# Performance work log

Measured on AMD Instinct MI355X. Metric: run time of the kernel, lower is better.

The kernel has to match this reference:

```python
import jax, jax.numpy as jnp
import numpy as np

B, N, C_IN, C_OUT, K = 8, 4096, 64, 128, 15
RADIUS = 0.1            # 2.5 * grid_size(0.04) * sigma(1.0)
MAX_NN = 34
KP_EXTENT = 0.04        # point_influence = prev_grid_size * sigma
KERNEL_RADIUS = 1.5 * KP_EXTENT
NEG_SLOPE = 0.2
BN_EPS = 1e-5


def setup_inputs() -> dict:
    key = jax.random.key(0)
    k1, k2, k3, k4 = jax.random.split(key, 4)
    xyz = jax.random.uniform(k1, (B, N, 3), dtype=jnp.float32)
    feats = jax.random.normal(k2, (B, N, C_IN), dtype=jnp.float32)
    # fixed kernel point disposition inside the kernel ball (requires_grad=False in torch)
    kp = jax.random.normal(k3, (K, 3), dtype=jnp.float32)
    kp = kp / (jnp.linalg.norm(kp, axis=-1, keepdims=True) + 1e-6) * KERNEL_RADIUS * 0.7
    kp = kp.at[0].set(0.0)  # center point
    std = float(np.sqrt(2.0 / (K * C_IN)))
    weight = jax.random.normal(k4, (K, C_IN, C_OUT), dtype=jnp.float32) * std
    gamma = jnp.ones((C_OUT,), dtype=jnp.float32)
    beta = jnp.zeros((C_OUT,), dtype=jnp.float32)
    return {"xyz": xyz, "feats": feats, "K_points": kp, "weight": weight,
            "gamma": gamma, "beta": beta}


def _ball_query(xyz):
    # xyz: [B, N, 3] -> flat neighbor idx [B*N, MAX_NN] into the concatenated
    # point array; missing neighbors get shadow index B*N.
    b_, n_, _ = xyz.shape
    shadow = b_ * n_

    def per_cloud(pts, b):
        d2 = jnp.sum((pts[:, None, :] - pts[None, :, :]) ** 2, axis=-1)  # [N, N]
        neg_d2, idx = jax.lax.top_k(-d2, MAX_NN)                         # k nearest
        valid = (-neg_d2) <= RADIUS ** 2
        return jnp.where(valid, idx + b * n_, shadow)

    return jax.vmap(per_cloud)(xyz, jnp.arange(b_)).reshape(b_ * n_, MAX_NN)


def _kpconv_block(xyz, feats, K_points, weight, gamma, beta):
    b_, n_, _ = xyz.shape
    pts = xyz.reshape(b_ * n_, 3)
    f = feats.reshape(b_ * n_, C_IN)
    nidx = _ball_query(xyz)                                   # [M, nn]
    # shadow point far away / zero features (KPConv_ops)
    pts_pad = jnp.concatenate([pts, jnp.full((1, 3), 1e6, pts.dtype)], axis=0)
    f_pad = jnp.concatenate([f, jnp.zeros((1, C_IN), f.dtype)], axis=0)
    nbr = pts_pad[nidx] - pts[:, None, :]                     # [M, nn, 3] relative coords
    sq = jnp.sum((nbr[:, :, None, :] - K_points) ** 2, -1)    # [M, nn, K]
    w = jnp.maximum(1.0 - jnp.sqrt(sq) / KP_EXTENT, 0.0)      # linear influence
    nf = f_pad[nidx]                                          # [M, nn, Cin]
    wf = jnp.einsum('mnk,mnc->mkc', w, nf)                    # per-kernel-point feats
    out = jnp.einsum('mkc,kcd->md', wf, weight)               # [M, Cout]
    # FastBatchNorm1d (training-mode batch stats, biased var) + LeakyReLU
    mu = out.mean(axis=0)
    var = out.var(axis=0)
    out = (out - mu) * jax.lax.rsqrt(var + BN_EPS) * gamma + beta
    out = jnp.where(out >= 0, out, NEG_SLOPE * out)
    return out.reshape(b_, n_, C_OUT)


def reference(xyz, feats, K_points, weight, gamma, beta):
    return _kpconv_block(xyz, feats, K_points, weight, gamma, beta)
```

## Files before the change

kernel.cpp:

```cpp
#include <hip/hip_runtime.h>


#define NB     8
#define NPTS   4096
#define M_TOT  32768
#define CIN    64
#define COUT   128
#define NKP    15
#define NCELL  1728
#define UCAP   400
#define R2EFF  (0.082f * 0.082f)
#define KP_INV 25.0f
#define NEG_SLOPE 0.2f
#define KCP    960
#define WFROW  1920
#define SP     40

typedef float f32x4_t __attribute__((ext_vector_type(4)));
typedef short bf16x8_t __attribute__((ext_vector_type(8)));

__device__ __forceinline__ unsigned short f2bf(float f) {
  union { float f; unsigned u; } v; v.f = f;
  unsigned r = v.u + 0x7FFF + ((v.u >> 16) & 1);
  return (unsigned short)(r >> 16);
}
__device__ __forceinline__ unsigned short f2bf_fast(float f) {
  union { float f; unsigned u; } v; v.f = f;
  return (unsigned short)((v.u + 0x8000u) >> 16);
}
__device__ __forceinline__ int cell_of(float x, float y, float z) {
  int cx = (int)(x * 12.f); cx = cx > 11 ? 11 : cx;
  int cy = (int)(y * 12.f); cy = cy > 11 ? 11 : cy;
  int cz = (int)(z * 12.f); cz = cz > 11 ? 11 : cz;
  return (cz * 12 + cy) * 12 + cx;
}

__global__ __launch_bounds__(256) void k0a_hist(
    const float* __restrict__ xyz, int* __restrict__ cellcnt)
{
  const int pt = blockIdx.x * 256 + threadIdx.x;
  const float x = xyz[pt * 3], y = xyz[pt * 3 + 1], z = xyz[pt * 3 + 2];
  const int b = pt >> 12;
  atomicAdd(&cellcnt[b * NCELL + cell_of(x, y, z)], 1);
}

__global__ __launch_bounds__(256) void k0b_scan_kW(
    const int* __restrict__ cellcnt, int* __restrict__ cellstart,
    const float* __restrict__ W, unsigned short* __restrict__ Wt)
{
  if (blockIdx.x >= 8) {
    const int idx = (blockIdx.x - 8) * 256 + threadIdx.x;
    const int c = idx & 63, d = idx >> 6;
    #pragma unroll
    for (int k = 0; k < NKP; k++)
      Wt[(size_t)d * KCP + k * 64 + c] =
          f2bf(W[(size_t)k * (CIN * COUT) + c * COUT + d]);
    return;
  }
  __shared__ int ps[256];
  const int b = blockIdx.x, t = threadIdx.x;
  int local[7], s = 0;
  #pragma unroll
  for (int i = 0; i < 7; i++) {
    const int cid = t * 7 + i;
    const int c = (cid < NCELL) ? cellcnt[b * NCELL + cid] : 0;
    local[i] = c; s += c;
  }
  ps[t] = s; __syncthreads();
  for (int off = 1; off < 256; off <<= 1) {
    int v = (t >= off) ? ps[t - off] : 0;
    __syncthreads();
    ps[t] += v;
    __syncthreads();
  }
  int run = ps[t] - s;
  #pragma unroll
  for (int i = 0; i < 7; i++) {
    const int cid = t * 7 + i;
    if (cid < NCELL) { cellstart[b * 1729 + cid] = run; run += local[i]; }
  }
  if (t == 255) cellstart[b * 1729 + NCELL] = ps[255];
}

__global__ __launch_bounds__(256) void k0c_scatter(
    const float* __restrict__ xyz, const float* __restrict__ feats,
    const int* __restrict__ cellstart, int* __restrict__ cellfill,
    int* __restrict__ qorder, float4* __restrict__ xyzs,
    unsigned short* __restrict__ fsorted)
{
  const int pt = blockIdx.x * 256 + threadIdx.x;
  const float x = xyz[pt * 3], y = xyz[pt * 3 + 1], z = xyz[pt * 3 + 2];
  const int b = pt >> 12;
  const int cid = cell_of(x, y, z);
  const int slot = atomicAdd(&cellfill[b * NCELL + cid], 1);
  const int pos = b * NPTS + cellstart[b * 1729 + cid] + slot;
  qorder[pos] = pt;
  xyzs[pos] = make_float4(x, y, z, 0.f);
  const float* src = &feats[(size_t)pt * CIN];
  uint4* dst = (uint4*)&fsorted[(size_t)pos * CIN];
  #pragma unroll
  for (int g = 0; g < 8; g++) {
    float4 a = *(const float4*)(src + g * 8);
    float4 c = *(const float4*)(src + g * 8 + 4);
    union { unsigned short s[8]; uint4 v; } u;
    u.s[0] = f2bf(a.x); u.s[1] = f2bf(a.y); u.s[2] = f2bf(a.z); u.s[3] = f2bf(a.w);
    u.s[4] = f2bf(c.x); u.s[5] = f2bf(c.y); u.s[6] = f2bf(c.z); u.s[7] = f2bf(c.w);
    dst[g] = u.v;
  }
}

__global__ __launch_bounds__(256, 5) void k2_conv(
    const float4* __restrict__ xyzs, const unsigned short* __restrict__ fsorted,
    const float* __restrict__ kpts, const int* __restrict__ cellstart,
    const int* __restrict__ qorder, const unsigned short* __restrict__ Wt,
    float* __restrict__ out, float* __restrict__ psum,
    float* __restrict__ psumsq)
{
  __shared__ char smraw[32000] __attribute__((aligned(16)));
  float4*         Pu   = (float4*)smraw;
  unsigned short* cpos = (unsigned short*)(smraw + 6400);
  short (*S)[SP]       = (short(*)[SP])(smraw + 6400);
  short (*FT)[SP]      = (short(*)[SP])(smraw + 26880);

  __shared__ float4 qd[16];
  __shared__ int    qm[16];
  __shared__ float  kp[NKP][4];
  __shared__ int    Tsh;
  __shared__ int    ucnt;

  const int tid = threadIdx.x;
  const int w   = tid >> 6;
  const int L   = tid & 63;
  const int m0  = blockIdx.x * 16;
  const int b   = m0 >> 12;

  if (tid >= 64 && tid < 64 + NKP) {
    const int k = tid - 64;
    const float kx = kpts[k * 3], ky = kpts[k * 3 + 1], kz = kpts[k * 3 + 2];
    kp[k][0] = -2.f * kx; kp[k][1] = -2.f * ky; kp[k][2] = -2.f * kz;
    kp[k][3] = kx * kx + ky * ky + kz * kz;
  }

  if (tid < 64) {
    int cxm = 12, cym = 12, czm = 12, cxM = -1, cyM = -1, czM = -1;
    if (tid < 16) {
      const float4 Q = xyzs[m0 + tid];
      qd[tid] = Q;
      qm[tid] = qorder[m0 + tid];
      int a = (int)(Q.x * 12.f); a = a > 11 ? 11 : a;
      int c = (int)(Q.y * 12.f); c = c > 11 ? 11 : c;
      int d = (int)(Q.z * 12.f); d = d > 11 ? 11 : d;
      cxm = cxM = a; cym = cyM = c; czm = czM = d;
    }
    #pragma unroll
    for (int off = 8; off >= 1; off >>= 1) {
      int v;
      v = __shfl_xor(cxm, off); cxm = v < cxm ? v : cxm;
      v = __shfl_xor(cxM, off); cxM = v > cxM ? v : cxM;
      v = __shfl_xor(cym, off); cym = v < cym ? v : cym;
      v = __shfl_xor(cyM, off); cyM = v > cyM ? v : cyM;
      v = __shfl_xor(czm, off); czm = v < czm ? v : czm;
      v = __shfl_xor(czM, off); czM = v > czM ? v : czM;
    }
    cxm = __shfl(cxm, 0); cxM = __shfl(cxM, 0);
    cym = __shfl(cym, 0); cyM = __shfl(cyM, 0);
    czm = __shfl(czm, 0); czM = __shfl(czM, 0);

    const int x0 = cxm > 0 ? cxm - 1 : 0, x1 = cxM < 11 ? cxM + 1 : 11;
    const int y0 = cym > 0 ? cym - 1 : 0, y1 = cyM < 11 ? cyM + 1 : 11;
    const int z0 = czm > 0 ? czm - 1 : 0, z1 = czM < 11 ? czM + 1 : 11;
    const int yspan = y1 - y0 + 1;
    int nr = yspan * (z1 - z0 + 1);
    nr = nr > 64 ? 64 : nr;

    int rs = 0, len = 0;
    if (tid < nr) {
      const int zz = z0 + tid / yspan, yy = y0 + tid % yspan;
      const int base = b * 1729 + (zz * 12 + yy) * 12;
      rs  = cellstart[base + x0];
      len = cellstart[base + x1 + 1] - rs;
    }
    int incl = len;
    #pragma unroll
    for (int off = 1; off < 64; off <<= 1) {
      const int v = __shfl_up(incl, off);
      if (tid >= off) incl += v;
    }
    const int excl = incl - len;
    for (int i = 0; i < len; i++) cpos[excl + i] = (unsigned short)(rs + i);
    if (tid == 63) Tsh = incl;
    if (tid == 62) ucnt = 0;
  }
  __syncthreads();
  const int T = Tsh;

  for (int tb = 0; tb < T; tb += 256) {
    const int t = tb + tid;
    if (t < T) {
      const int pos = (int)cpos[t];
      const float4 P = xyzs[b * NPTS + pos];
      float best = 1e9f;
      #pragma unroll
      for (int i = 0; i < 16; i++) {
        const float4 Q = qd[i];
        const float dx = P.x - Q.x, dy = P.y - Q.y, dz = P.z - Q.z;
        const float d2 = dx * dx + dy * dy + dz * dz;
        best = d2 < best ? d2 : best;
      }
      if (best <= R2EFF) {
        const int slot = atomicAdd(&ucnt, 1);
        if (slot < UCAP)
          Pu[slot] = make_float4(P.x, P.y, P.z, __int_as_float(pos));
      }
    }
  }
  __syncthreads();
  int U = ucnt; U = U > UCAP ? UCAP : U;

  const int ln = L & 15;
  const int kh = L >> 4;
  const int qh = tid >> 5;
  const int nn = tid & 31;

  f32x4_t acc[16];
  #pragma unroll
  for (int mt = 0; mt < 16; mt++) acc[mt] = (f32x4_t){0.f, 0.f, 0.f, 0.f};

  for (int ub = 0; ub < U; ub += 32) {
    {
      const int c  = tid & 63;
      const int i0 = tid >> 6;
      #pragma unroll
      for (int ii = 0; ii < 8; ii++) {
        const int i = ii * 4 + i0;
        const int u = ub + i;
        short v = 0;
        if (u < U) {
          const int pos = __float_as_int(Pu[u].w);
          v = (short)fsorted[(size_t)(b * NPTS + pos) * CIN + c];
        }
        FT[c][i] = v;
      }
    }

    bf16x8_t bb;
    #pragma unroll
    for (int half = 0; half < 2; half++) {
      {
        const int u = ub + nn;
        if (u < U) {
          const float4 P = Pu[u];
          const float4 Q = qd[half * 8 + qh];
          const float rx = P.x - Q.x, ry = P.y - Q.y, rz = P.z - Q.z;
          const float rr = rx * rx + ry * ry + rz * rz;
          #pragma unroll
          for (int k = 0; k < NKP; k++) {
            float d2 = fmaf(kp[k][0], rx,
                       fmaf(kp[k][1], ry,
                       fmaf(kp[k][2], rz, rr + kp[k][3])));
            d2 = fmaxf(d2, 0.f);
            const float wv =
                fmaxf(fmaf(-KP_INV, __builtin_amdgcn_sqrtf(d2), 1.f), 0.f);
            S[qh * 16 + k][nn] = (short)f2bf_fast(wv);
          }
          S[qh * 16 + 15][nn] = 0;
        } else {
          #pragma unroll
          for (int k = 0; k < 16; k++) S[qh * 16 + k][nn] = 0;
        }
      }
      __syncthreads();
      if (half == 0) bb = *(const bf16x8_t*)&FT[w * 16 + ln][kh * 8];
      #pragma unroll
      for (int mt = 0; mt < 8; mt++) {
        bf16x8_t aa = *(const bf16x8_t*)&S[mt * 16 + ln][kh * 8];
        acc[half * 8 + mt] =
            __builtin_amdgcn_mfma_f32_16x16x32_bf16(aa, bb, acc[half * 8 + mt],
                                                    0, 0, 0);
      }
      __syncthreads();
    }
  }

  {
    const int c = w * 16 + ln;
    #pragma unroll
    for (int mt = 0; mt < 16; mt++) {
      #pragma unroll
      for (int j = 0; j < 4; j++) {
        const int k = kh * 4 + j;
        if (k < 15) {
          int byteo = mt * WFROW + ((k * 64 + c) << 1);
          byteo ^= (mt & 7) << 4;
          *(unsigned short*)(smraw + byteo) = f2bf_fast(acc[mt][j]);
        }
      }
    }
  }
  __syncthreads();

  const int colbase = w * 32;

  f32x4_t acc2[2];
  acc2[0] = (f32x4_t){0.f, 0.f, 0.f, 0.f};
  acc2[1] = (f32x4_t){0.f, 0.f, 0.f, 0.f};

  const unsigned short* Bp0 = &Wt[(size_t)(colbase + ln) * KCP + kh * 8];
  const unsigned short* Bp1 = Bp0 + 16 * KCP;
  const char* wfb = (const char*)smraw + ln * WFROW;
  const int   sw  = (ln & 7) << 4;

  #pragma unroll 6
  for (int kk = 0; kk < 30; kk++) {
    const int ko  = kk * 32;
    const int inr = (kh * 16 + kk * 64) ^ sw;
    bf16x8_t b0 = *(const bf16x8_t*)(Bp0 + ko);
    bf16x8_t b1 = *(const bf16x8_t*)(Bp1 + ko);
    bf16x8_t a0 = *(const bf16x8_t*)(wfb + inr);
    acc2[0] = __builtin_amdgcn_mfma_f32_16x16x32_bf16(a0, b0, acc2[0], 0, 0, 0);
    acc2[1] = __builtin_amdgcn_mfma_f32_16x16x32_bf16(a0, b1, acc2[1], 0, 0, 0);
  }

  float s0 = 0.f, q0 = 0.f, s1 = 0.f, q1 = 0.f;
  #pragma unroll
  for (int j = 0; j < 4; j++) {
    s0 += acc2[0][j]; q0 += acc2[0][j] * acc2[0][j];
    s1 += acc2[1][j]; q1 += acc2[1][j] * acc2[1][j];
  }
  s0 += __shfl_xor(s0, 16); s0 += __shfl_xor(s0, 32);
  q0 += __shfl_xor(q0, 16); q0 += __shfl_xor(q0, 32);
  s1 += __shfl_xor(s1, 16); s1 += __shfl_xor(s1, 32);
  q1 += __shfl_xor(q1, 16); q1 += __shfl_xor(q1, 32);
  if (kh == 0) {
    atomicAdd(&psum[colbase + ln], s0);
    atomicAdd(&psumsq[colbase + ln], q0);
    atomicAdd(&psum[colbase + 16 + ln], s1);
    atomicAdd(&psumsq[colbase + 16 + ln], q1);
  }

  #pragma unroll
  for (int c = 0; c < 2; c++) {
    #pragma unroll
    for (int j = 0; j < 4; j++) {
      const int row = kh * 4 + j;
      out[(size_t)qm[row] * COUT + colbase + c * 16 + ln] = acc2[c][j];
    }
  }
}

__global__ __launch_bounds__(256) void k4_norm(
    float* __restrict__ out, const float* __restrict__ psum,
    const float* __restrict__ psumsq, const float* __restrict__ gamma,
    const float* __restrict__ beta)
{
  __shared__ float a_s[128], b_s[128];
  if (threadIdx.x < 128) {
    const int d = threadIdx.x;
    double mu  = (double)psum[d] / (double)M_TOT;
    double var = (double)psumsq[d] / (double)M_TOT - mu * mu;
    float rstd = (float)(1.0 / sqrt(var + 1e-5));
    float a = rstd * gamma[d];
    a_s[d] = a;
    b_s[d] = beta[d] - (float)mu * a;
  }
  __syncthreads();
  const int idx = blockIdx.x * 256 + threadIdx.x;
  float4 v = ((const float4*)out)[idx];
  const int d0 = (idx * 4) & 127;
  float y0 = v.x * a_s[d0 + 0] + b_s[d0 + 0];
  float y1 = v.y * a_s[d0 + 1] + b_s[d0 + 1];
  float y2 = v.z * a_s[d0 + 2] + b_s[d0 + 2];
  float y3 = v.w * a_s[d0 + 3] + b_s[d0 + 3];
  v.x = y0 >= 0.f ? y0 : NEG_SLOPE * y0;
  v.y = y1 >= 0.f ? y1 : NEG_SLOPE * y1;
  v.z = y2 >= 0.f ? y2 : NEG_SLOPE * y2;
  v.w = y3 >= 0.f ? y3 : NEG_SLOPE * y3;
  ((float4*)out)[idx] = v;
}

extern "C" void kernel_launch(void* const* d_in, const int* in_sizes, int n_in,
                              void* d_out, int out_size, void* d_ws,
                              size_t ws_size, hipStream_t stream)
{
  const float* xyz   = (const float*)d_in[0];
  const float* feats = (const float*)d_in[1];
  const float* kpts  = (const float*)d_in[2];
  const float* W     = (const float*)d_in[3];
  const float* gamma = (const float*)d_in[4];
  const float* beta  = (const float*)d_in[5];
  float* out = (float*)d_out;

  char* ws = (char*)d_ws;
  int*            cellcnt   = (int*)(ws + 0);
  int*            cellfill  = (int*)(ws + 55296);
  float*          psum      = (float*)(ws + 110592);
  float*          psumsq    = (float*)(ws + 111104);
  int*            cellstart = (int*)(ws + 111616);
  int*            qorder    = (int*)(ws + 167040);
  float4*         xyzs      = (float4*)(ws + 298112);
  unsigned short* fsorted   = (unsigned short*)(ws + 822400);
  unsigned short* Wt        = (unsigned short*)(ws + 5016704);

  hipMemsetAsync(ws, 0, 111616, stream);

  k0a_hist   <<< 128, 256, 0, stream>>>(xyz, cellcnt);
  k0b_scan_kW<<<  40, 256, 0, stream>>>(cellcnt, cellstart, W, Wt);
  k0c_scatter<<< 128, 256, 0, stream>>>(xyz, feats, cellstart, cellfill,
                                        qorder, xyzs, fsorted);
  k2_conv    <<<2048, 256, 0, stream>>>(xyzs, fsorted, kpts, cellstart,
                                        qorder, Wt, out, psum, psumsq);
  k4_norm    <<<(out_size / 4) / 256, 256, 0, stream>>>(out, psum, psumsq,
                                                        gamma, beta);
}
```

Measured before the change: 195.9 us.

## Prefetch neighbor features into registers, aggregate atomics per wave, swizzle block order

The block index is remapped so that consecutive blocks come from different clouds, spreading spatial work across the GPU. The per-thread shared atomicAdd in candidate compaction is replaced by a wave-level ballot with one atomic per wave and a popcount-based slot. The feature gather for the next 32-point chunk is issued into registers before the current chunk's compute runs, so its global-load latency can overlap with the MFMA work. This costs extra registers, which could lower occupancy.

```diff
diff --git a/kernel.cpp b/kernel.cpp
--- a/kernel.cpp
+++ b/kernel.cpp
@@ -131,7 +131,8 @@
   const int tid = threadIdx.x;
   const int w   = tid >> 6;
   const int L   = tid & 63;
-  const int m0  = blockIdx.x * 16;
+  const int tile = ((blockIdx.x & 7) << 8) | (blockIdx.x >> 3);
+  const int m0  = tile * 16;
   const int b   = m0 >> 12;
 
   if (tid >= 64 && tid < 64 + NKP) {
@@ -196,9 +197,12 @@
 
   for (int tb = 0; tb < T; tb += 256) {
     const int t = tb + tid;
+    bool hit = false;
+    float4 P;
+    int pos = 0;
     if (t < T) {
-      const int pos = (int)cpos[t];
-      const float4 P = xyzs[b * NPTS + pos];
+      pos = (int)cpos[t];
+      P = xyzs[b * NPTS + pos];
       float best = 1e9f;
       #pragma unroll
       for (int i = 0; i < 16; i++) {
@@ -207,8 +211,17 @@
         const float d2 = dx * dx + dy * dy + dz * dz;
         best = d2 < best ? d2 : best;
       }
-      if (best <= R2EFF) {
-        const int slot = atomicAdd(&ucnt, 1);
+      hit = best <= R2EFF;
+    }
+    const unsigned long long m = __ballot(hit);
+    if (m) {
+      const int cnt = __popcll(m);
+      const int leader = __ffsll((long long)m) - 1;
+      int base = 0;
+      if (L == leader) base = atomicAdd(&ucnt, cnt);
+      base = __shfl(base, leader);
+      if (hit) {
+        const int slot = base + __popcll(m & ((1ull << L) - 1ull));
         if (slot < UCAP)
           Pu[slot] = make_float4(P.x, P.y, P.z, __int_as_float(pos));
       }
@@ -221,25 +234,40 @@
   const int kh = L >> 4;
   const int qh = tid >> 5;
   const int nn = tid & 31;
+  const int gc  = tid & 63;
+  const int gi0 = tid >> 6;
 
   f32x4_t acc[16];
   #pragma unroll
   for (int mt = 0; mt < 16; mt++) acc[mt] = (f32x4_t){0.f, 0.f, 0.f, 0.f};
 
+  short pv[8];
+  #pragma unroll
+  for (int ii = 0; ii < 8; ii++) {
+    const int u = ii * 4 + gi0;
+    short v = 0;
+    if (u < U) {
+      const int pos = __float_as_int(Pu[u].w);
+      v = (short)fsorted[(size_t)(b * NPTS + pos) * CIN + gc];
+    }
+    pv[ii] = v;
+  }
+
   for (int ub = 0; ub < U; ub += 32) {
-    {
-      const int c  = tid & 63;
-      const int i0 = tid >> 6;
+    #pragma unroll
+    for (int ii = 0; ii < 8; ii++) FT[gc][ii * 4 + gi0] = pv[ii];
+
+    const int ubn = ub + 32;
+    if (ubn < U) {
       #pragma unroll
       for (int ii = 0; ii < 8; ii++) {
-        const int i = ii * 4 + i0;
-        const int u = ub + i;
+        const int u = ubn + ii * 4 + gi0;
         short v = 0;
         if (u < U) {
           const int pos = __float_as_int(Pu[u].w);
-          v = (short)fsorted[(size_t)(b * NPTS + pos) * CIN + c];
+          v = (short)fsorted[(size_t)(b * NPTS + pos) * CIN + gc];
         }
-        FT[c][i] = v;
+        pv[ii] = v;
       }
     }
 
```

Result: no change. 194.9 us (-0.5%).

## Give each wave its own 4 queries with private neighbor lists and MFMA tiles

Applied to the files above, without the earlier changes.

Restructures the conv kernel so each wave owns 4 query points. Each wave gathers its own candidate neighbors with ballot/popcount compaction instead of shared atomics, and runs the weight and feature MFMA tiles in private LDS without block-wide barriers inside the neighbor loop. This removes the per-chunk __syncthreads and the shared union of all 16 queries, which can shrink the per-query candidate set. In exchange, LDS per block grows to 48KB, occupancy drops to 3 blocks per SIMD, and the neighbor scan is repeated per wave. Candidates are capped at 128 per wave, which risks truncation.

```diff
diff --git a/kernel.cpp b/kernel.cpp
--- a/kernel.cpp
+++ b/kernel.cpp
@@ -8,13 +8,14 @@
 #define COUT   128
 #define NKP    15
 #define NCELL  1728
-#define UCAP   400
+#define UCAP4  128
 #define R2EFF  (0.082f * 0.082f)
 #define KP_INV 25.0f
 #define NEG_SLOPE 0.2f
 #define KCP    960
 #define WFROW  1920
 #define SP     40
+#define WSTRIDE 12288
 
 typedef float f32x4_t __attribute__((ext_vector_type(4)));
 typedef short bf16x8_t __attribute__((ext_vector_type(8)));
@@ -33,6 +34,9 @@
   int cy = (int)(y * 12.f); cy = cy > 11 ? 11 : cy;
   int cz = (int)(z * 12.f); cz = cz > 11 ? 11 : cz;
   return (cz * 12 + cy) * 12 + cx;
+}
+__device__ __forceinline__ int cix(float v) {
+  int c = (int)(v * 12.f); return c > 11 ? 11 : c;
 }
 
 __global__ __launch_bounds__(256) void k0a_hist(
@@ -109,24 +113,15 @@
   }
 }
 
-__global__ __launch_bounds__(256, 5) void k2_conv(
+__global__ __launch_bounds__(256, 3) void k2_conv(
     const float4* __restrict__ xyzs, const unsigned short* __restrict__ fsorted,
     const float* __restrict__ kpts, const int* __restrict__ cellstart,
     const int* __restrict__ qorder, const unsigned short* __restrict__ Wt,
     float* __restrict__ out, float* __restrict__ psum,
     float* __restrict__ psumsq)
 {
-  __shared__ char smraw[32000] __attribute__((aligned(16)));
-  float4*         Pu   = (float4*)smraw;
-  unsigned short* cpos = (unsigned short*)(smraw + 6400);
-  short (*S)[SP]       = (short(*)[SP])(smraw + 6400);
-  short (*FT)[SP]      = (short(*)[SP])(smraw + 26880);
-
-  __shared__ float4 qd[16];
-  __shared__ int    qm[16];
-  __shared__ float  kp[NKP][4];
-  __shared__ int    Tsh;
-  __shared__ int    ucnt;
+  __shared__ char smraw[49152] __attribute__((aligned(16)));
+  __shared__ int qm[16];
 
   const int tid = threadIdx.x;
   const int w   = tid >> 6;
@@ -134,165 +129,159 @@
   const int m0  = blockIdx.x * 16;
   const int b   = m0 >> 12;
 
-  if (tid >= 64 && tid < 64 + NKP) {
-    const int k = tid - 64;
-    const float kx = kpts[k * 3], ky = kpts[k * 3 + 1], kz = kpts[k * 3 + 2];
-    kp[k][0] = -2.f * kx; kp[k][1] = -2.f * ky; kp[k][2] = -2.f * kz;
-    kp[k][3] = kx * kx + ky * ky + kz * kz;
-  }
-
-  if (tid < 64) {
-    int cxm = 12, cym = 12, czm = 12, cxM = -1, cyM = -1, czM = -1;
-    if (tid < 16) {
-      const float4 Q = xyzs[m0 + tid];
-      qd[tid] = Q;
-      qm[tid] = qorder[m0 + tid];
-      int a = (int)(Q.x * 12.f); a = a > 11 ? 11 : a;
-      int c = (int)(Q.y * 12.f); c = c > 11 ? 11 : c;
-      int d = (int)(Q.z * 12.f); d = d > 11 ? 11 : d;
-      cxm = cxM = a; cym = cyM = c; czm = czM = d;
-    }
-    #pragma unroll
-    for (int off = 8; off >= 1; off >>= 1) {
-      int v;
-      v = __shfl_xor(cxm, off); cxm = v < cxm ? v : cxm;
-      v = __shfl_xor(cxM, off); cxM = v > cxM ? v : cxM;
-      v = __shfl_xor(cym, off); cym = v < cym ? v : cym;
-      v = __shfl_xor(cyM, off); cyM = v > cyM ? v : cyM;
-      v = __shfl_xor(czm, off); czm = v < czm ? v : czm;
-      v = __shfl_xor(czM, off); czM = v > czM ? v : czM;
-    }
-    cxm = __shfl(cxm, 0); cxM = __shfl(cxM, 0);
-    cym = __shfl(cym, 0); cyM = __shfl(cyM, 0);
-    czm = __shfl(czm, 0); czM = __shfl(czM, 0);
-
-    const int x0 = cxm > 0 ? cxm - 1 : 0, x1 = cxM < 11 ? cxM + 1 : 11;
-    const int y0 = cym > 0 ? cym - 1 : 0, y1 = cyM < 11 ? cyM + 1 : 11;
-    const int z0 = czm > 0 ? czm - 1 : 0, z1 = czM < 11 ? czM + 1 : 11;
-    const int yspan = y1 - y0 + 1;
-    int nr = yspan * (z1 - z0 + 1);
-    nr = nr > 64 ? 64 : nr;
-
-    int rs = 0, len = 0;
-    if (tid < nr) {
-      const int zz = z0 + tid / yspan, yy = y0 + tid % yspan;
-      const int base = b * 1729 + (zz * 12 + yy) * 12;
-      rs  = cellstart[base + x0];
-      len = cellstart[base + x1 + 1] - rs;
-    }
-    int incl = len;
-    #pragma unroll
-    for (int off = 1; off < 64; off <<= 1) {
-      const int v = __shfl_up(incl, off);
-      if (tid >= off) incl += v;
-    }
-    const int excl = incl - len;
-    for (int i = 0; i < len; i++) cpos[excl + i] = (unsigned short)(rs + i);
-    if (tid == 63) Tsh = incl;
-    if (tid == 62) ucnt = 0;
-  }
-  __syncthreads();
-  const int T = Tsh;
-
-  for (int tb = 0; tb < T; tb += 256) {
-    const int t = tb + tid;
-    if (t < T) {
-      const int pos = (int)cpos[t];
-      const float4 P = xyzs[b * NPTS + pos];
-      float best = 1e9f;
-      #pragma unroll
-      for (int i = 0; i < 16; i++) {
-        const float4 Q = qd[i];
-        const float dx = P.x - Q.x, dy = P.y - Q.y, dz = P.z - Q.z;
-        const float d2 = dx * dx + dy * dy + dz * dz;
-        best = d2 < best ? d2 : best;
+  char* wbase = smraw + w * WSTRIDE;
+  short (*S)[SP]  = (short(*)[SP])wbase;
+  short (*FT)[SP] = (short(*)[SP])(wbase + 5120);
+  float4* Pu      = (float4*)(wbase + 10240);
+
+  const int kk_ = L & 15;
+  float k2x = 0.f, k2y = 0.f, k2z = 0.f, kpc = 0.f;
+  if (kk_ < NKP) {
+    const float kx = kpts[kk_ * 3], ky = kpts[kk_ * 3 + 1],
+                kz = kpts[kk_ * 3 + 2];
+    k2x = -2.f * kx; k2y = -2.f * ky; k2z = -2.f * kz;
+    kpc = kx * kx + ky * ky + kz * kz;
+  }
+
+  const int q0g = m0 + w * 4;
+  if (L < 4) qm[w * 4 + L] = qorder[q0g + L];
+  const float4 Q0 = xyzs[q0g + 0];
+  const float4 Q1 = xyzs[q0g + 1];
+  const float4 Q2 = xyzs[q0g + 2];
+  const float4 Q3 = xyzs[q0g + 3];
+  const float4 Qs = xyzs[q0g + (L >> 4)];
+
+  int cxm = cix(Q0.x), cxM = cxm, cym = cix(Q0.y), cyM = cym,
+      czm = cix(Q0.z), czM = czm;
+  {
+    int v;
+    v = cix(Q1.x); cxm = v < cxm ? v : cxm; cxM = v > cxM ? v : cxM;
+    v = cix(Q2.x); cxm = v < cxm ? v : cxm; cxM = v > cxM ? v : cxM;
+    v = cix(Q3.x); cxm = v < cxm ? v : cxm; cxM = v > cxM ? v : cxM;
+    v = cix(Q1.y); cym = v < cym ? v : cym; cyM = v > cyM ? v : cyM;
+    v = cix(Q2.y); cym = v < cym ? v : cym; cyM = v > cyM ? v : cyM;
+    v = cix(Q3.y); cym = v < cym ? v : cym; cyM = v > cyM ? v : cyM;
+    v = cix(Q1.z); czm = v < czm ? v : czm; czM = v > czM ? v : czM;
+    v = cix(Q2.z); czm = v < czm ? v : czm; czM = v > czM ? v : czM;
+    v = cix(Q3.z); czm = v < czm ? v : czm; czM = v > czM ? v : czM;
+  }
+  const int x0 = cxm > 0 ? cxm - 1 : 0, x1 = cxM < 11 ? cxM + 1 : 11;
+  const int y0 = cym > 0 ? cym - 1 : 0, y1 = cyM < 11 ? cyM + 1 : 11;
+  const int z0 = czm > 0 ? czm - 1 : 0, z1 = czM < 11 ? czM + 1 : 11;
+  const int yspan = y1 - y0 + 1;
+  int nr = yspan * (z1 - z0 + 1);
+  nr = nr > 64 ? 64 : nr;
+
+  int rs = 0, re = 0;
+  if (L < nr) {
+    const int zz = z0 + L / yspan, yy = y0 + L % yspan;
+    const int base = b * 1729 + (zz * 12 + yy) * 12;
+    rs = cellstart[base + x0];
+    re = cellstart[base + x1 + 1];
+  }
+
+  int cnt = 0;
+  for (int r = 0; r < nr; r++) {
+    const int rrs = __shfl(rs, r), rre = __shfl(re, r);
+    for (int t0 = rrs; t0 < rre; t0 += 64) {
+      const int t = t0 + L;
+      bool hit = false;
+      float4 P;
+      if (t < rre) {
+        P = xyzs[b * NPTS + t];
+        float dx = P.x - Q0.x, dy = P.y - Q0.y, dz = P.z - Q0.z;
+        float best = dx * dx + dy * dy + dz * dz;
+        dx = P.x - Q1.x; dy = P.y - Q1.y; dz = P.z - Q1.z;
+        float d2 = dx * dx + dy * dy + dz * dz; best = d2 < best ? d2 : best;
+        dx = P.x - Q2.x; dy = P.y - Q2.y; dz = P.z - Q2.z;
+        d2 = dx * dx + dy * dy + dz * dz; best = d2 < best ? d2 : best;
+        dx = P.x - Q3.x; dy = P.y - Q3.y; dz = P.z - Q3.z;
+        d2 = dx * dx + dy * dy + dz * dz; best = d2 < best ? d2 : best;
+        hit = best <= R2EFF;
       }
-      if (best <= R2EFF) {
-        const int slot = atomicAdd(&ucnt, 1);
-        if (slot < UCAP)
-          Pu[slot] = make_float4(P.x, P.y, P.z, __int_as_float(pos));
+      const unsigned long long m = __ballot(hit);
+      if (hit) {
+        const int slot = cnt + __popcll(m & ((1ull << L) - 1ull));
+        if (slot < UCAP4)
+          Pu[slot] = make_float4(P.x, P.y, P.z, __int_as_float(t));
       }
-    }
-  }
-  __syncthreads();
-  int U = ucnt; U = U > UCAP ? UCAP : U;
+      cnt += __popcll(m);
+    }
+  }
+  int U = cnt > UCAP4 ? UCAP4 : cnt;
 
   const int ln = L & 15;
   const int kh = L >> 4;
-  const int qh = tid >> 5;
-  const int nn = tid & 31;
-
-  f32x4_t acc[16];
-  #pragma unroll
-  for (int mt = 0; mt < 16; mt++) acc[mt] = (f32x4_t){0.f, 0.f, 0.f, 0.f};
+
+  f32x4_t acc[4][4];
+  #pragma unroll
+  for (int mt = 0; mt < 4; mt++)
+    #pragma unroll
+    for (int nt = 0; nt < 4; nt++)
+      acc[mt][nt] = (f32x4_t){0.f, 0.f, 0.f, 0.f};
 
   for (int ub = 0; ub < U; ub += 32) {
     {
-      const int c  = tid & 63;
-      const int i0 = tid >> 6;
+      union { unsigned short s[32]; uint4 v[4]; } fu;
       #pragma unroll
-      for (int ii = 0; ii < 8; ii++) {
-        const int i = ii * 4 + i0;
-        const int u = ub + i;
-        short v = 0;
-        if (u < U) {
-          const int pos = __float_as_int(Pu[u].w);
-          v = (short)fsorted[(size_t)(b * NPTS + pos) * CIN + c];
-        }
-        FT[c][i] = v;
+      for (int n = 0; n < 32; n++) {
+        const int u = ub + n;
+        const int uu = u < U ? u : U - 1;
+        const int pos = __float_as_int(Pu[uu].w);
+        unsigned short v = 0;
+        if (u < U) v = fsorted[(size_t)(b * NPTS + pos) * CIN + L];
+        fu.s[n] = v;
       }
-    }
-
-    bf16x8_t bb;
-    #pragma unroll
-    for (int half = 0; half < 2; half++) {
-      {
-        const int u = ub + nn;
-        if (u < U) {
-          const float4 P = Pu[u];
-          const float4 Q = qd[half * 8 + qh];
-          const float rx = P.x - Q.x, ry = P.y - Q.y, rz = P.z - Q.z;
-          const float rr = rx * rx + ry * ry + rz * rz;
-          #pragma unroll
-          for (int k = 0; k < NKP; k++) {
-            float d2 = fmaf(kp[k][0], rx,
-                       fmaf(kp[k][1], ry,
-                       fmaf(kp[k][2], rz, rr + kp[k][3])));
-            d2 = fmaxf(d2, 0.f);
-            const float wv =
-                fmaxf(fmaf(-KP_INV, __builtin_amdgcn_sqrtf(d2), 1.f), 0.f);
-            S[qh * 16 + k][nn] = (short)f2bf_fast(wv);
-          }
-          S[qh * 16 + 15][nn] = 0;
-        } else {
-          #pragma unroll
-          for (int k = 0; k < 16; k++) S[qh * 16 + k][nn] = 0;
-        }
+      uint4* dst = (uint4*)&FT[L][0];
+      dst[0] = fu.v[0]; dst[1] = fu.v[1]; dst[2] = fu.v[2]; dst[3] = fu.v[3];
+    }
+    {
+      union { unsigned short s[32]; uint4 v[4]; } su;
+      #pragma unroll
+      for (int n = 0; n < 32; n++) {
+        const int u = ub + n;
+        const int uu = u < U ? u : U - 1;
+        const float4 P = Pu[uu];
+        const float rx = P.x - Qs.x, ry = P.y - Qs.y, rz = P.z - Qs.z;
+        const float rr = rx * rx + ry * ry + rz * rz;
+        float d2 = fmaf(k2x, rx, fmaf(k2y, ry, fmaf(k2z, rz, rr + kpc)));
+        d2 = fmaxf(d2, 0.f);
+        const float wv =
+            fmaxf(fmaf(-KP_INV, __builtin_amdgcn_sqrtf(d2), 1.f), 0.f);
+        su.s[n] = (u < U && kk_ < NKP) ? f2bf_fast(wv) : (unsigned short)0;
       }
-      __syncthreads();
-      if (half == 0) bb = *(const bf16x8_t*)&FT[w * 16 + ln][kh * 8];
+      uint4* dst = (uint4*)&S[L][0];
+      dst[0] = su.v[0]; dst[1] = su.v[1]; dst[2] = su.v[2]; dst[3] = su.v[3];
+    }
+    bf16x8_t aa[4], bb[4];
+    #pragma unroll
+    for (int i = 0; i < 4; i++) {
+      aa[i] = *(const bf16x8_t*)&S[i * 16 + ln][kh * 8];
+      bb[i] = *(const bf16x8_t*)&FT[i * 16 + ln][kh * 8];
+    }
+    #pragma unroll
+    for (int mt = 0; mt < 4; mt++)
       #pragma unroll
-      for (int mt = 0; mt < 8; mt++) {
-        bf16x8_t aa = *(const bf16x8_t*)&S[mt * 16 + ln][kh * 8];
-        acc[half * 8 + mt] =
-            __builtin_amdgcn_mfma_f32_16x16x32_bf16(aa, bb, acc[half * 8 + mt],
-                                                    0, 0, 0);
-      }
-      __syncthreads();
-    }
-  }
-
-  {
-    const int c = w * 16 + ln;
-    #pragma unroll
-    for (int mt = 0; mt < 16; mt++) {
+      for (int nt = 0; nt < 4; nt++)
+        acc[mt][nt] = __builtin_amdgcn_mfma_f32_16x16x32_bf16(
+            aa[mt], bb[nt], acc[mt][nt], 0, 0, 0);
+  }
+
+  __syncthreads();
+
+  #pragma unroll
+  for (int mt = 0; mt < 4; mt++) {
+    const int row = w * 4 + mt;
+    const int swz = (row & 7) << 4;
+    #pragma unroll
+    for (int nt = 0; nt < 4; nt++) {
+      const int c = nt * 16 + ln;
       #pragma unroll
       for (int j = 0; j < 4; j++) {
         const int k = kh * 4 + j;
         if (k < 15) {
-          int byteo = mt * WFROW + ((k * 64 + c) << 1);
-          byteo ^= (mt & 7) << 4;
-          *(unsigned short*)(smraw + byteo) = f2bf_fast(acc[mt][j]);
+          const int byteo = (row * WFROW + ((k * 64 + c) << 1)) ^ swz;
+          *(unsigned short*)(smraw + byteo) = f2bf_fast(acc[mt][nt][j]);
         }
       }
     }
```

After: 203.8 us. +4.0%, slower.

## Halve query tile to 8 points per block and restructure weight computation

Applied to the files above, without the earlier changes.

The conv kernel now handles 8 query points per block instead of 16. It launches twice as many blocks, interleaved across batches, uses less shared memory and allows higher occupancy. The kernel-point weight tile is now computed with each thread owning one (query, kernel point) row and writing 16 entries with vector stores, with one barrier per neighbor chunk instead of two. Candidate compaction uses a wave-aggregated atomic. The trade-offs are fewer query points sharing each gathered neighbor set, so more total gather and candidate-scan work, and a second GEMM that wastes half its MFMA rows.

```diff
diff --git a/kernel.cpp b/kernel.cpp
--- a/kernel.cpp
+++ b/kernel.cpp
@@ -8,6 +8,7 @@
 #define COUT   128
 #define NKP    15
 #define NCELL  1728
+#define QB     8
 #define UCAP   400
 #define R2EFF  (0.082f * 0.082f)
 #define KP_INV 25.0f
@@ -109,21 +110,21 @@
   }
 }
 
-__global__ __launch_bounds__(256, 5) void k2_conv(
+__global__ __launch_bounds__(256, 6) void k2_conv(
     const float4* __restrict__ xyzs, const unsigned short* __restrict__ fsorted,
     const float* __restrict__ kpts, const int* __restrict__ cellstart,
     const int* __restrict__ qorder, const unsigned short* __restrict__ Wt,
     float* __restrict__ out, float* __restrict__ psum,
     float* __restrict__ psumsq)
 {
-  __shared__ char smraw[32000] __attribute__((aligned(16)));
+  __shared__ char smraw[21760] __attribute__((aligned(16)));
   float4*         Pu   = (float4*)smraw;
   unsigned short* cpos = (unsigned short*)(smraw + 6400);
   short (*S)[SP]       = (short(*)[SP])(smraw + 6400);
-  short (*FT)[SP]      = (short(*)[SP])(smraw + 26880);
-
-  __shared__ float4 qd[16];
-  __shared__ int    qm[16];
+  short (*FT)[SP]      = (short(*)[SP])(smraw + 16640);
+
+  __shared__ float4 qd[QB];
+  __shared__ int    qm[QB];
   __shared__ float  kp[NKP][4];
   __shared__ int    Tsh;
   __shared__ int    ucnt;
@@ -131,8 +132,9 @@
   const int tid = threadIdx.x;
   const int w   = tid >> 6;
   const int L   = tid & 63;
-  const int m0  = blockIdx.x * 16;
-  const int b   = m0 >> 12;
+  const int tile = ((blockIdx.x & 7) << 9) | (blockIdx.x >> 3);
+  const int m0  = tile * QB;
+  const int b   = blockIdx.x & 7;
 
   if (tid >= 64 && tid < 64 + NKP) {
     const int k = tid - 64;
@@ -143,7 +145,7 @@
 
   if (tid < 64) {
     int cxm = 12, cym = 12, czm = 12, cxM = -1, cyM = -1, czM = -1;
-    if (tid < 16) {
+    if (tid < QB) {
       const float4 Q = xyzs[m0 + tid];
       qd[tid] = Q;
       qm[tid] = qorder[m0 + tid];
@@ -153,7 +155,7 @@
       cxm = cxM = a; cym = cyM = c; czm = czM = d;
     }
     #pragma unroll
-    for (int off = 8; off >= 1; off >>= 1) {
+    for (int off = 4; off >= 1; off >>= 1) {
       int v;
       v = __shfl_xor(cxm, off); cxm = v < cxm ? v : cxm;
       v = __shfl_xor(cxM, off); cxM = v > cxM ? v : cxM;
@@ -196,19 +198,31 @@
 
   for (int tb = 0; tb < T; tb += 256) {
     const int t = tb + tid;
+    bool hit = false;
+    float4 P;
+    int pos = 0;
     if (t < T) {
-      const int pos = (int)cpos[t];
-      const float4 P = xyzs[b * NPTS + pos];
+      pos = (int)cpos[t];
+      P = xyzs[b * NPTS + pos];
       float best = 1e9f;
       #pragma unroll
-      for (int i = 0; i < 16; i++) {
+      for (int i = 0; i < QB; i++) {
         const float4 Q = qd[i];
         const float dx = P.x - Q.x, dy = P.y - Q.y, dz = P.z - Q.z;
         const float d2 = dx * dx + dy * dy + dz * dz;
         best = d2 < best ? d2 : best;
       }
-      if (best <= R2EFF) {
-        const int slot = atomicAdd(&ucnt, 1);
+      hit = best <= R2EFF;
+    }
+    const unsigned long long m = __ballot(hit);
+    if (m) {
+      const int cnt = __popcll(m);
+      const int leader = __ffsll((long long)m) - 1;
+      int base2 = 0;
+      if (L == leader) base2 = atomicAdd(&ucnt, cnt);
+      base2 = __shfl(base2, leader);
+      if (hit) {
+        const int slot = base2 + __popcll(m & ((1ull << L) - 1ull));
         if (slot < UCAP)
           Pu[slot] = make_float4(P.x, P.y, P.z, __int_as_float(pos));
       }
@@ -219,14 +233,22 @@
 
   const int ln = L & 15;
   const int kh = L >> 4;
-  const int qh = tid >> 5;
-  const int nn = tid & 31;
-
-  f32x4_t acc[16];
-  #pragma unroll
-  for (int mt = 0; mt < 16; mt++) acc[mt] = (f32x4_t){0.f, 0.f, 0.f, 0.f};
+  const int sr   = tid >> 1;
+  const int sh16 = (tid & 1) << 4;
+  const int sq   = sr >> 4;
+  const int sk   = sr & 15;
+  const float4 Qt = qd[sq];
+  float k2x = 0.f, k2y = 0.f, k2z = 0.f, kpc = 0.f;
+  if (sk < NKP) {
+    k2x = kp[sk][0]; k2y = kp[sk][1]; k2z = kp[sk][2]; kpc = kp[sk][3];
+  }
+
+  f32x4_t acc[QB];
+  #pragma unroll
+  for (int mt = 0; mt < QB; mt++) acc[mt] = (f32x4_t){0.f, 0.f, 0.f, 0.f};
 
   for (int ub = 0; ub < U; ub += 32) {
+    if (ub) __syncthreads();
     {
       const int c  = tid & 63;
       const int i0 = tid >> 6;
@@ -242,56 +264,45 @@
         FT[c][i] = v;
       }
     }
-
-    bf16x8_t bb;
-    #pragma unroll
-    for (int half = 0; half < 2; half++) {
-      {
-        const int u = ub + nn;
-        if (u < U) {
-          const float4 P = Pu[u];
-          const float4 Q = qd[half * 8 + qh];
-          const float rx = P.x - Q.x, ry = P.y - Q.y, rz = P.z - Q.z;
-          const float rr = rx * rx + ry * ry + rz * rz;
-          #pragma unroll
-          for (int k = 0; k < NKP; k++) {
-            float d2 = fmaf(kp[k][0], rx,
-                       fmaf(kp[k][1], ry,
-                       fmaf(kp[k][2], rz, rr + kp[k][3])));
-            d2 = fmaxf(d2, 0.f);
-            const float wv =
-                fmaxf(fmaf(-KP_INV, __builtin_amdgcn_sqrtf(d2), 1.f), 0.f);
-            S[qh * 16 + k][nn] = (short)f2bf_fast(wv);
-          }
-          S[qh * 16 + 15][nn] = 0;
-        } else {
-          #pragma unroll
-          for (int k = 0; k < 16; k++) S[qh * 16 + k][nn] = 0;
-        }
+    {
+      union { unsigned short s[16]; uint4 v[2]; } su;
+      #pragma unroll
+      for (int n = 0; n < 16; n++) {
+        const int u = ub + sh16 + n;
+        const int uu = u < U ? u : 0;
+        const float4 P = Pu[uu];
+        const float rx = P.x - Qt.x, ry = P.y - Qt.y, rz = P.z - Qt.z;
+        const float rr = rx * rx + ry * ry + rz * rz;
+        float d2 = fmaf(k2x, rx, fmaf(k2y, ry, fmaf(k2z, rz, rr + kpc)));
+        d2 = fmaxf(d2, 0.f);
+        const float wv =
+            fmaxf(fmaf(-KP_INV, __builtin_amdgcn_sqrtf(d2), 1.f), 0.f);
+        su.s[n] = (u < U && sk < NKP) ? f2bf_fast(wv) : (unsigned short)0;
       }
-      __syncthreads();
-      if (half == 0) bb = *(const bf16x8_t*)&FT[w * 16 + ln][kh * 8];
-      #pragma unroll
-      for (int mt = 0; mt < 8; mt++) {
-        bf16x8_t aa = *(const bf16x8_t*)&S[mt * 16 + ln][kh * 8];
-        acc[half * 8 + mt] =
-            __builtin_amdgcn_mfma_f32_16x16x32_bf16(aa, bb, acc[half * 8 + mt],
-                                                    0, 0, 0);
-      }
-      __syncthreads();
-    }
-  }
+      uint4* dst = (uint4*)&S[sr][sh16];
+      dst[0] = su.v[0]; dst[1] = su.v[1];
+    }
+    __syncthreads();
+
+    bf16x8_t bb = *(const bf16x8_t*)&FT[w * 16 + ln][kh * 8];
+    #pragma unroll
+    for (int mt = 0; mt < QB; mt++) {
+      bf16x8_t aa = *(const bf16x8_t*)&S[mt * 16 + ln][kh * 8];
+      acc[mt] = __builtin_amdgcn_mfma_f32_16x16x32_bf16(aa, bb, acc[mt],
+                                                        0, 0, 0);
+    }
+  }
+  __syncthreads();
 
   {
     const int c = w * 16 + ln;
     #pragma unroll
-    for (int mt = 0; mt < 16; mt++) {
+    for (int mt = 0; mt < QB; mt++) {
       #pragma unroll
       for (int j = 0; j < 4; j++) {
         const int k = kh * 4 + j;
         if (k < 15) {
-          int byteo = mt * WFROW + ((k * 64 + c) << 1);
-          byteo ^= (mt & 7) << 4;
+          const int byteo = (mt * WFROW + ((k * 64 + c) << 1)) ^ (mt << 4);
           *(unsigned short*)(smraw + byteo) = f2bf_fast(acc[mt][j]);
         }
       }
@@ -309,6 +320,7 @@
   const unsigned short* Bp1 = Bp0 + 16 * KCP;
   const char* wfb = (const char*)smraw + ln * WFROW;
   const int   sw  = (ln & 7) << 4;
+  const bool  arow = ln < QB;
 
   #pragma unroll 6
   for (int kk = 0; kk < 30; kk++) {
@@ -316,7 +328,8 @@
     const int inr = (kh * 16 + kk * 64) ^ sw;
     bf16x8_t b0 = *(const bf16x8_t*)(Bp0 + ko);
     bf16x8_t b1 = *(const bf16x8_t*)(Bp1 + ko);
-    bf16x8_t a0 = *(const bf16x8_t*)(wfb + inr);
+    bf16x8_t a0 = (bf16x8_t){0, 0, 0, 0, 0, 0, 0, 0};
+    if (arow) a0 = *(const bf16x8_t*)(wfb + inr);
     acc2[0] = __builtin_amdgcn_mfma_f32_16x16x32_bf16(a0, b0, acc2[0], 0, 0, 0);
     acc2[1] = __builtin_amdgcn_mfma_f32_16x16x32_bf16(a0, b1, acc2[1], 0, 0, 0);
   }
@@ -343,7 +356,8 @@
     #pragma unroll
     for (int j = 0; j < 4; j++) {
       const int row = kh * 4 + j;
-      out[(size_t)qm[row] * COUT + colbase + c * 16 + ln] = acc2[c][j];
+      if (row < QB)
+        out[(size_t)qm[row] * COUT + colbase + c * 16 + ln] = acc2[c][j];
     }
   }
 }
@@ -407,7 +421,7 @@
   k0b_scan_kW<<<  40, 256, 0, stream>>>(cellcnt, cellstart, W, Wt);
   k0c_scatter<<< 128, 256, 0, stream>>>(xyz, feats, cellstart, cellfill,
                                         qorder, xyzs, fsorted);
-  k2_conv    <<<2048, 256, 0, stream>>>(xyzs, fsorted, kpts, cellstart,
+  k2_conv    <<<4096, 256, 0, stream>>>(xyzs, fsorted, kpts, cellstart,
                                         qorder, Wt, out, psum, psumsq);
   k4_norm    <<<(out_size / 4) / 256, 256, 0, stream>>>(out, psum, psumsq,
                                                         gamma, beta);
```

New measurement: 240.7 us. +22.9%, slower.
